# Kernel tuning notes

Hardware: AMD Instinct MI355X
Metric: run time of the kernel (lower is better)

The kernel has to match this reference:

```python
import jax, jax.numpy as jnp
jax.config.update("jax_enable_x64", True)
import numpy as np
import math

N = 100_000   # number of events
D = 4         # feature dim
M = 256       # number of Gaussian centers
E = 10        # ensemble size
SIGMA = 0.1
NORM_CONST = 1.0 / ((2.0 * math.pi) ** (D / 2) * SIGMA ** D)


def setup_inputs() -> dict:
    key = jax.random.key(0)
    k = jax.random.split(key, 6)
    x = jax.random.normal(k[0], (N, D), dtype=jnp.float64)
    centers = jax.random.normal(k[1], (M, D), dtype=jnp.float64)
    coefficients = jax.random.normal(k[2], (M,), dtype=jnp.float64)
    ensemble_probs = jax.random.uniform(k[3], (N, E), dtype=jnp.float64)
    ensemble_norm_probs = jax.random.uniform(k[4], (N, 1), dtype=jnp.float64)
    # small positive weights so 1 - sum(w) stays positive (as in a fitted model)
    weights = 0.05 * jax.random.uniform(k[5], (E,), dtype=jnp.float64)
    return {
        "x": x,
        "ensemble_probs": ensemble_probs,
        "ensemble_norm_probs": ensemble_norm_probs,
        "weights": weights,
        "centers": centers,
        "coefficients": coefficients,
    }


def reference(x, ensemble_probs, ensemble_norm_probs, weights, centers, coefficients):
    # GaussianKernelLayer.get_kernels: pairwise squared distances -> RBF
    diff = x[:, None, :] - centers[None, :, :]          # [N, M, D]
    dist_sq = jnp.sum(diff * diff, axis=2)              # [N, M]
    kern = NORM_CONST * jnp.exp(-0.5 * dist_sq / (SIGMA ** 2))  # [N, M]
    # centered coefficients, contract: einsum('m,Nm->N')
    wc = coefficients - coefficients.mean()
    net_out = kern @ wc                                 # [N]
    # ensemble mixture: w [E,1], w_norm [1,1]
    w = weights[:, None]
    w_norm = 1.0 - jnp.sum(w, axis=0, keepdims=True)
    ensemble = ensemble_probs @ w + ensemble_norm_probs @ w_norm  # [N, 1]
    return (ensemble, net_out)
```

## Files before the change

kernel.cpp:

```cpp
#include <hip/hip_runtime.h>
#include <math.h>

#define NROWS 100000
#define MCENT 256
#define EENS 10

#define NORM_CONST_F 253.30295910584444f
#define EXP2_SCALE (-72.13475204444817f)

#define DROP_T 0.30f

__global__ __launch_bounds__(256) void fused_kernel(
    const float* __restrict__ x,
    const float* __restrict__ ensemble_probs,
    const float* __restrict__ ensemble_norm_probs,
    const float* __restrict__ weights,
    const float* __restrict__ centers,
    const float* __restrict__ coefficients,
    float* __restrict__ out)
{
    __shared__ float s_p1[4][64];
    __shared__ float s_p2[4][64];

    const int t = threadIdx.x;
    const int lane = t & 63;
    const int wid = __builtin_amdgcn_readfirstlane(t >> 6);

    const int r = blockIdx.x * 64 + lane;
    const int rc = (r < NROWS) ? r : (NROWS - 1);

    const float4 xv = ((const float4*)x)[rc];

    const float4* __restrict__ C = (const float4*)centers + wid * 64;
    const float*  __restrict__ K = coefficients + wid * 64;

    float a1 = 0.f;
    float a2 = 0.f;

    #pragma unroll 4
    for (int k = 0; k < 64; ++k) {
        const float4 c = C[k];
        const float dx = xv.x - c.x, dy = xv.y - c.y,
                    dz = xv.z - c.z, dw = xv.w - c.w;
        float d2 = dx * dx;
        d2 = fmaf(dy, dy, d2);
        d2 = fmaf(dz, dz, d2);
        d2 = fmaf(dw, dw, d2);
        if (__any(d2 < DROP_T)) {
            const float e = __builtin_amdgcn_exp2f(d2 * EXP2_SCALE);
            a1 = fmaf(K[k], e, a1);
            a2 += e;
        }
    }

    s_p1[wid][lane] = a1;
    s_p2[wid][lane] = a2;
    __syncthreads();

    if (wid == 0) {
        const float4 cf4 = ((const float4*)coefficients)[lane];
        float s = (cf4.x + cf4.y) + (cf4.z + cf4.w);
        #pragma unroll
        for (int off = 32; off > 0; off >>= 1) s += __shfl_down(s, off, 64);
        const float mean = __builtin_amdgcn_readfirstlane(s) * (1.0f / 256.0f);

        if (r < NROWS) {
            const float P1 = (s_p1[0][lane] + s_p1[1][lane]) +
                             (s_p1[2][lane] + s_p1[3][lane]);
            const float P2 = (s_p2[0][lane] + s_p2[1][lane]) +
                             (s_p2[2][lane] + s_p2[3][lane]);
            out[NROWS + r] = (P1 - mean * P2) * NORM_CONST_F;
        }
    } else if (wid == 1) {
        if (r < NROWS) {
            float wv[EENS];
            float wsum = 0.0f;
            #pragma unroll
            for (int e = 0; e < EENS; ++e) { wv[e] = weights[e]; wsum += wv[e]; }
            float ens = ensemble_norm_probs[r] * (1.0f - wsum);
            const float2* pr = (const float2*)(ensemble_probs + (size_t)r * EENS);
            #pragma unroll
            for (int e2 = 0; e2 < EENS / 2; ++e2) {
                const float2 p = pr[e2];
                ens = fmaf(p.x, wv[2 * e2 + 0], ens);
                ens = fmaf(p.y, wv[2 * e2 + 1], ens);
            }
            out[r] = ens;
        }
    }
}

extern "C" void kernel_launch(void* const* d_in, const int* in_sizes, int n_in,
                              void* d_out, int out_size, void* d_ws, size_t ws_size,
                              hipStream_t stream) {
    const float* x       = (const float*)d_in[0];
    const float* eprobs  = (const float*)d_in[1];
    const float* enorm   = (const float*)d_in[2];
    const float* weights = (const float*)d_in[3];
    const float* centers = (const float*)d_in[4];
    const float* coeffs  = (const float*)d_in[5];
    float* out = (float*)d_out;

    const int blocks = (NROWS + 63) / 64;
    fused_kernel<<<blocks, 256, 0, stream>>>(
        x, eprobs, enorm, weights, centers, coeffs, out);
}
```

Before: 13.71 us.

## Compute pairwise distances via split-f16 MFMA dot products instead of scalar loops

Expands squared distance as |x|^2+|c|^2-2x·c and computes the cross term with 16x16x32 f16 MFMA. Centers are split into hi/lo f16 parts and x into hi or lo per lane group to keep near-fp32 accuracy. Each wave handles 32 rows against all 256 centers and reduces with shuffles, which removes the shared-memory reduction and __syncthreads. The mean is now folded into per-center coefficients, and exp work is skipped per wave when every exponent argument is below a threshold. This trades VALU distance math for matrix-core work plus extra register pressure from keeping all center fragments in registers.

```diff
diff --git a/kernel.cpp b/kernel.cpp
--- a/kernel.cpp
+++ b/kernel.cpp
@@ -2,15 +2,18 @@
 #include <math.h>
 
 #define NROWS 100000
-#define MCENT 256
 #define EENS 10
 
 #define NORM_CONST_F 253.30295910584444f
 #define EXP2_SCALE (-72.13475204444817f)
+#define M2_CONST   (144.26950408889634f)
+#define ARG_THRESH (-18.0f)
 
-#define DROP_T 0.30f
+typedef _Float16 h8 __attribute__((ext_vector_type(8)));
+typedef float    f4 __attribute__((ext_vector_type(4)));
 
-__global__ __launch_bounds__(256) void fused_kernel(
+
+__global__ __launch_bounds__(512, 1) void fused_kernel(
     const float* __restrict__ x,
     const float* __restrict__ ensemble_probs,
     const float* __restrict__ ensemble_norm_probs,
@@ -19,74 +22,161 @@
     const float* __restrict__ coefficients,
     float* __restrict__ out)
 {
-    __shared__ float s_p1[4][64];
-    __shared__ float s_p2[4][64];
+    const int t    = threadIdx.x;
+    const int lane = t & 63;
+    const int wid  = t >> 6;
+    const int wg   = blockIdx.x * 8 + wid;
+    if (wg >= NROWS / 32) return;
+    const int wbase = wg * 32;
 
-    const int t = threadIdx.x;
-    const int lane = t & 63;
-    const int wid = __builtin_amdgcn_readfirstlane(t >> 6);
+    const int lr = lane & 15;
+    const int g  = lane >> 4;
 
-    const int r = blockIdx.x * 64 + lane;
-    const int rc = (r < NROWS) ? r : (NROWS - 1);
+    const float4 cq = ((const float4*)coefficients)[lane];
+    float ms = (cq.x + cq.y) + (cq.z + cq.w);
+    #pragma unroll
+    for (int off = 32; off > 0; off >>= 1) ms += __shfl_down(ms, off, 64);
+    const float mean = __builtin_amdgcn_readfirstlane(ms) * (1.0f / 256.0f);
 
-    const float4 xv = ((const float4*)x)[rc];
+    h8 bf[16]; float As[16], wcv[16];
+    #pragma unroll
+    for (int T = 0; T < 16; ++T) {
+        const float4 cv = ((const float4*)centers)[T * 16 + lr];
+        const _Float16 h0 = (_Float16)cv.x, h1 = (_Float16)cv.y,
+                       h2 = (_Float16)cv.z, h3 = (_Float16)cv.w;
+        const _Float16 l0 = (_Float16)(cv.x - (float)h0),
+                       l1 = (_Float16)(cv.y - (float)h1),
+                       l2 = (_Float16)(cv.z - (float)h2),
+                       l3 = (_Float16)(cv.w - (float)h3);
+        h8 b;
+        b[0] = h0; b[1] = h1; b[2] = h2; b[3] = h3;
+        b[4] = l0; b[5] = l1; b[6] = l2; b[7] = l3;
+        bf[T] = b;
+        float n2 = cv.x * cv.x;
+        n2 = fmaf(cv.y, cv.y, n2);
+        n2 = fmaf(cv.z, cv.z, n2);
+        n2 = fmaf(cv.w, cv.w, n2);
+        As[T]  = EXP2_SCALE * n2;
+        wcv[T] = coefficients[T * 16 + lr] - mean;
+    }
 
-    const float4* __restrict__ C = (const float4*)centers + wid * 64;
-    const float*  __restrict__ K = coefficients + wid * 64;
+    const float4 xa = ((const float4*)x)[wbase + lr];
+    const float4 xb = ((const float4*)x)[wbase + 16 + lr];
 
-    float a1 = 0.f;
-    float a2 = 0.f;
+    float hsa = xa.x * xa.x;
+    hsa = fmaf(xa.y, xa.y, hsa); hsa = fmaf(xa.z, xa.z, hsa); hsa = fmaf(xa.w, xa.w, hsa);
+    hsa *= EXP2_SCALE;
+    float hsb = xb.x * xb.x;
+    hsb = fmaf(xb.y, xb.y, hsb); hsb = fmaf(xb.z, xb.z, hsb); hsb = fmaf(xb.w, xb.w, hsb);
+    hsb *= EXP2_SCALE;
 
-    #pragma unroll 4
-    for (int k = 0; k < 64; ++k) {
-        const float4 c = C[k];
-        const float dx = xv.x - c.x, dy = xv.y - c.y,
-                    dz = xv.z - c.z, dw = xv.w - c.w;
-        float d2 = dx * dx;
-        d2 = fmaf(dy, dy, d2);
-        d2 = fmaf(dz, dz, d2);
-        d2 = fmaf(dw, dw, d2);
-        if (__any(d2 < DROP_T)) {
-            const float e = __builtin_amdgcn_exp2f(d2 * EXP2_SCALE);
-            a1 = fmaf(K[k], e, a1);
-            a2 += e;
+    const float HA0 = __shfl(hsa, g * 4 + 0, 64), HA1 = __shfl(hsa, g * 4 + 1, 64),
+                HA2 = __shfl(hsa, g * 4 + 2, 64), HA3 = __shfl(hsa, g * 4 + 3, 64);
+    const float HB0 = __shfl(hsb, g * 4 + 0, 64), HB1 = __shfl(hsb, g * 4 + 1, 64),
+                HB2 = __shfl(hsb, g * 4 + 2, 64), HB3 = __shfl(hsb, g * 4 + 3, 64);
+
+    const float a0f = (float)(_Float16)xa.x, a1f = (float)(_Float16)xa.y,
+                a2f = (float)(_Float16)xa.z, a3f = (float)(_Float16)xa.w;
+    const float b0f = (float)(_Float16)xb.x, b1f = (float)(_Float16)xb.y,
+                b2f = (float)(_Float16)xb.z, b3f = (float)(_Float16)xb.w;
+
+    const float sa0 = (g == 0) ? a0f : (g == 1) ? (xa.x - a0f) : 0.f;
+    const float sa1 = (g == 0) ? a1f : (g == 1) ? (xa.y - a1f) : 0.f;
+    const float sa2 = (g == 0) ? a2f : (g == 1) ? (xa.z - a2f) : 0.f;
+    const float sa3 = (g == 0) ? a3f : (g == 1) ? (xa.w - a3f) : 0.f;
+    const float sb0 = (g == 0) ? b0f : (g == 1) ? (xb.x - b0f) : 0.f;
+    const float sb1 = (g == 0) ? b1f : (g == 1) ? (xb.y - b1f) : 0.f;
+    const float sb2 = (g == 0) ? b2f : (g == 1) ? (xb.z - b2f) : 0.f;
+    const float sb3 = (g == 0) ? b3f : (g == 1) ? (xb.w - b3f) : 0.f;
+
+    h8 afA, afB;
+    afA[0] = (_Float16)sa0; afA[1] = (_Float16)sa1; afA[2] = (_Float16)sa2; afA[3] = (_Float16)sa3;
+    afA[4] = afA[0]; afA[5] = afA[1]; afA[6] = afA[2]; afA[7] = afA[3];
+    afB[0] = (_Float16)sb0; afB[1] = (_Float16)sb1; afB[2] = (_Float16)sb2; afB[3] = (_Float16)sb3;
+    afB[4] = afB[0]; afB[5] = afB[1]; afB[6] = afB[2]; afB[7] = afB[3];
+
+    f4 accA = {0.f, 0.f, 0.f, 0.f};
+    f4 accB = {0.f, 0.f, 0.f, 0.f};
+    const f4 z4 = {0.f, 0.f, 0.f, 0.f};
+
+    #pragma unroll
+    for (int T = 0; T < 16; ++T) {
+        const f4 dA = __builtin_amdgcn_mfma_f32_16x16x32_f16(afA, bf[T], z4, 0, 0, 0);
+        const f4 dB = __builtin_amdgcn_mfma_f32_16x16x32_f16(afB, bf[T], z4, 0, 0, 0);
+
+        const float baseA = As[T];
+        const float ra0 = fmaf(M2_CONST, dA[0], HA0 + baseA);
+        const float ra1 = fmaf(M2_CONST, dA[1], HA1 + baseA);
+        const float ra2 = fmaf(M2_CONST, dA[2], HA2 + baseA);
+        const float ra3 = fmaf(M2_CONST, dA[3], HA3 + baseA);
+        const float mxa = fmaxf(fmaxf(ra0, ra1), fmaxf(ra2, ra3));
+        if (__any(mxa > ARG_THRESH)) {
+            const float e0 = __builtin_amdgcn_exp2f(ra0);
+            const float e1 = __builtin_amdgcn_exp2f(ra1);
+            const float e2 = __builtin_amdgcn_exp2f(ra2);
+            const float e3 = __builtin_amdgcn_exp2f(ra3);
+            accA[0] = fmaf(e0, wcv[T], accA[0]);
+            accA[1] = fmaf(e1, wcv[T], accA[1]);
+            accA[2] = fmaf(e2, wcv[T], accA[2]);
+            accA[3] = fmaf(e3, wcv[T], accA[3]);
+        }
+
+        const float rb0 = fmaf(M2_CONST, dB[0], HB0 + baseA);
+        const float rb1 = fmaf(M2_CONST, dB[1], HB1 + baseA);
+        const float rb2 = fmaf(M2_CONST, dB[2], HB2 + baseA);
+        const float rb3 = fmaf(M2_CONST, dB[3], HB3 + baseA);
+        const float mxb = fmaxf(fmaxf(rb0, rb1), fmaxf(rb2, rb3));
+        if (__any(mxb > ARG_THRESH)) {
+            const float e0 = __builtin_amdgcn_exp2f(rb0);
+            const float e1 = __builtin_amdgcn_exp2f(rb1);
+            const float e2 = __builtin_amdgcn_exp2f(rb2);
+            const float e3 = __builtin_amdgcn_exp2f(rb3);
+            accB[0] = fmaf(e0, wcv[T], accB[0]);
+            accB[1] = fmaf(e1, wcv[T], accB[1]);
+            accB[2] = fmaf(e2, wcv[T], accB[2]);
+            accB[3] = fmaf(e3, wcv[T], accB[3]);
         }
     }
 
-    s_p1[wid][lane] = a1;
-    s_p2[wid][lane] = a2;
-    __syncthreads();
+    #pragma unroll
+    for (int msk = 1; msk <= 8; msk <<= 1) {
+        accA[0] += __shfl_xor(accA[0], msk, 64);
+        accA[1] += __shfl_xor(accA[1], msk, 64);
+        accA[2] += __shfl_xor(accA[2], msk, 64);
+        accA[3] += __shfl_xor(accA[3], msk, 64);
+        accB[0] += __shfl_xor(accB[0], msk, 64);
+        accB[1] += __shfl_xor(accB[1], msk, 64);
+        accB[2] += __shfl_xor(accB[2], msk, 64);
+        accB[3] += __shfl_xor(accB[3], msk, 64);
+    }
+    if (lr == 0) {
+        const int rbA = wbase + g * 4;
+        out[NROWS + rbA + 0] = accA[0] * NORM_CONST_F;
+        out[NROWS + rbA + 1] = accA[1] * NORM_CONST_F;
+        out[NROWS + rbA + 2] = accA[2] * NORM_CONST_F;
+        out[NROWS + rbA + 3] = accA[3] * NORM_CONST_F;
+        const int rbB = rbA + 16;
+        out[NROWS + rbB + 0] = accB[0] * NORM_CONST_F;
+        out[NROWS + rbB + 1] = accB[1] * NORM_CONST_F;
+        out[NROWS + rbB + 2] = accB[2] * NORM_CONST_F;
+        out[NROWS + rbB + 3] = accB[3] * NORM_CONST_F;
+    }
 
-    if (wid == 0) {
-        const float4 cf4 = ((const float4*)coefficients)[lane];
-        float s = (cf4.x + cf4.y) + (cf4.z + cf4.w);
+    if (lane < 32) {
+        const int r = wbase + lane;
+        float wv[EENS];
+        float wsum = 0.0f;
         #pragma unroll
-        for (int off = 32; off > 0; off >>= 1) s += __shfl_down(s, off, 64);
-        const float mean = __builtin_amdgcn_readfirstlane(s) * (1.0f / 256.0f);
-
-        if (r < NROWS) {
-            const float P1 = (s_p1[0][lane] + s_p1[1][lane]) +
-                             (s_p1[2][lane] + s_p1[3][lane]);
-            const float P2 = (s_p2[0][lane] + s_p2[1][lane]) +
-                             (s_p2[2][lane] + s_p2[3][lane]);
-            out[NROWS + r] = (P1 - mean * P2) * NORM_CONST_F;
+        for (int e = 0; e < EENS; ++e) { wv[e] = weights[e]; wsum += wv[e]; }
+        float ens = ensemble_norm_probs[r] * (1.0f - wsum);
+        const float2* pr = (const float2*)(ensemble_probs + (size_t)r * EENS);
+        #pragma unroll
+        for (int e2 = 0; e2 < EENS / 2; ++e2) {
+            const float2 p = pr[e2];
+            ens = fmaf(p.x, wv[2 * e2 + 0], ens);
+            ens = fmaf(p.y, wv[2 * e2 + 1], ens);
         }
-    } else if (wid == 1) {
-        if (r < NROWS) {
-            float wv[EENS];
-            float wsum = 0.0f;
-            #pragma unroll
-            for (int e = 0; e < EENS; ++e) { wv[e] = weights[e]; wsum += wv[e]; }
-            float ens = ensemble_norm_probs[r] * (1.0f - wsum);
-            const float2* pr = (const float2*)(ensemble_probs + (size_t)r * EENS);
-            #pragma unroll
-            for (int e2 = 0; e2 < EENS / 2; ++e2) {
-                const float2 p = pr[e2];
-                ens = fmaf(p.x, wv[2 * e2 + 0], ens);
-                ens = fmaf(p.y, wv[2 * e2 + 1], ens);
-            }
-            out[r] = ens;
-        }
+        out[r] = ens;
     }
 }
 
@@ -101,7 +191,8 @@
     const float* coeffs  = (const float*)d_in[5];
     float* out = (float*)d_out;
 
-    const int blocks = (NROWS + 63) / 64;
-    fused_kernel<<<blocks, 256, 0, stream>>>(
+    const int waves  = NROWS / 32;
+    const int blocks = (waves + 7) / 8;
+    fused_kernel<<<blocks, 512, 0, stream>>>(
         x, eprobs, enorm, weights, centers, coeffs, out);
 }
```

New measurement: 13.93 us. No clear change (+1.6%).
